# Kernel optimization log

Measured on AMD Instinct MI355X. Metric: run time of the kernel, lower is better.

The kernel has to match this reference:

```python
import jax, jax.numpy as jnp
import numpy as np

B, Q, C = 64, 512, 128   # batch, num_queries, num_activity_classes
P, G = 2048, 256         # num_persons, num_target_groups
COST_BCE = 1.0
COST_ACT = 1.0


def setup_inputs() -> dict:
    key = jax.random.key(0)
    k1, k2, k3, k4 = jax.random.split(key, 4)
    pred_activity_logits = jax.random.normal(k1, (B, Q, C), dtype=jnp.float32)
    attention_weights = jax.random.normal(k2, (B, P, Q), dtype=jnp.float32)
    # binary one-hot-style grouping targets (~each person in 1-of-G groups; sparse 0/1)
    tgt_one_hot = (jax.random.uniform(k3, (B, P, G)) < (1.0 / G) * 8).astype(jnp.float32)
    tgt_activity_ids = jax.random.randint(k4, (B, G), 0, C, dtype=jnp.int64)
    return {
        "pred_activity_logits": pred_activity_logits,
        "attention_weights": attention_weights,
        "tgt_one_hot": tgt_one_hot,
        "tgt_activity_ids": tgt_activity_ids,
    }


def reference(pred_activity_logits, attention_weights, tgt_one_hot, tgt_activity_ids):
    """Fused cost-matrix computation.

    BCEWithLogits(x, t) (mean reduction) = mean(softplus(x) - x * t).
    grouping_cost[b,i,j] = mean_p BCE(attw[b,p,i], onehot[b,p,j])
                         = mean_p softplus(attw[b,p,i]) - (1/P) sum_p attw[b,p,i]*onehot[b,p,j]
    activity_cost[b,i,j] = mean_c BCE(logits[b,i,c], onehot(ids[b,j])[c])
                         = mean_c softplus(logits[b,i,c]) - (1/C) * logits[b,i,ids[b,j]]
    Returns the [B, Q, G] cost tensor (scipy linear_sum_assignment, which consumes
    it on CPU, is outside the kernel scope).
    """
    attw = attention_weights            # [B, P, Q]
    logits = pred_activity_logits       # [B, Q, C]
    p = attw.shape[1]
    c = logits.shape[2]

    # grouping (BCE) cost
    sp_g = jnp.mean(jax.nn.softplus(attw), axis=1)               # [B, Q]
    xt = jnp.einsum('bpq,bpg->bqg', attw, tgt_one_hot) / p       # [B, Q, G]
    grouping_cost = sp_g[:, :, None] - xt                        # [B, Q, G]

    # activity (BCE vs one-hot class) cost
    sp_a = jnp.mean(jax.nn.softplus(logits), axis=2)             # [B, Q]
    idx = jnp.broadcast_to(tgt_activity_ids[:, None, :], (logits.shape[0], logits.shape[1], tgt_activity_ids.shape[1]))
    gathered = jnp.take_along_axis(logits, idx.astype(jnp.int32), axis=2)  # [B, Q, G]
    activity_cost = sp_a[:, :, None] - gathered / c              # [B, Q, G]

    cost = COST_BCE * grouping_cost + COST_ACT * activity_cost
    return cost
```

## Files before the change

### kernel.cpp

```cpp
#include <hip/hip_runtime.h>
#include <hip/hip_bf16.h>

#define B_  64
#define Q_  512
#define C_  128
#define P_  2048
#define G_  256
#define BM  128
#define BN  256
#define BK  64
#define NT  512

typedef __attribute__((ext_vector_type(8))) short short8;
typedef __attribute__((ext_vector_type(4))) float floatx4;

union FragU { uint4 u; short8 s; };

__device__ __forceinline__ float bf2f(unsigned short h) {
    union { unsigned int i; float f; } v; v.i = ((unsigned int)h) << 16; return v.f;
}
__device__ __forceinline__ unsigned int f2bf(float f) {
    union { float f; unsigned int u; } v; v.f = f;
    return (v.u + 0x7FFFu + ((v.u >> 16) & 1u)) >> 16;
}
__device__ __forceinline__ float splus(float x) {
    return fmaxf(x, 0.f) + __logf(1.f + __expf(-fabsf(x)));
}
__device__ __forceinline__ void unpack8(float4 a, float4 b, float* c) {
    c[0] = a.x; c[1] = a.y; c[2] = a.z; c[3] = a.w;
    c[4] = b.x; c[5] = b.y; c[6] = b.z; c[7] = b.w;
}

__global__ __launch_bounds__(NT, 2)
void fused_cost_kernel(const float* __restrict__ logits,
                       const float* __restrict__ attw,
                       const float* __restrict__ onehot,
                       const int* __restrict__ ids,
                       float* __restrict__ out)
{
    __shared__ unsigned short smem[(BM + BN) * BK];
    __shared__ float spq[BM];
    __shared__ int idt[BN];
    __shared__ int sflags;
    unsigned short* As = smem;
    unsigned short* Bs = smem + BM * BK;

    const int tid = threadIdx.x;
    const int l   = tid & 63;
    const int w   = tid >> 6;
    const int wm  = w & 1;
    const int wn  = w >> 1;
    const int lm  = l & 15;
    const int lk  = l >> 4;

    const int nb = blockIdx.x * BN;
    const int mb = blockIdx.y * BM;
    const int b  = blockIdx.z;

    if (tid < BM) spq[tid] = 0.f;
    if (tid == 0) sflags = 0;
    __syncthreads();
    if (tid < 128) { if (ids[2 * tid + 1] != 0) atomicOr(&sflags, 1); }
    __syncthreads();
    const bool ids32 = (sflags & 1) != 0;
    if (tid < BN) {
        const int gidx = b * G_ + nb + tid;
        idt[tid] = ids32 ? ids[gidx] : ids[2 * gidx];
    }

    const int mvA = tid & 15;
    const int kqA = tid >> 4;
    const int hbA = kqA >> 2;
    const int kdA = kqA & 3;
    const int mvB = tid & 31;
    const int kqB = tid >> 5;
    const int hbB = kqB >> 1;
    const int sdB = (kqB & 1) * 4;

    const float* aSrc = attw   + (size_t)b * P_ * Q_ + (size_t)(2 * kqA) * Q_ + (mb + 8 * mvA);
    const float* bSrc = onehot + (size_t)b * P_ * G_ + (size_t)(4 * kqB) * G_ + (nb + 8 * mvB);

    float spacc[8] = {0.f, 0.f, 0.f, 0.f, 0.f, 0.f, 0.f, 0.f};
    floatx4 acc[4][4];
    #pragma unroll
    for (int mi = 0; mi < 4; ++mi)
        #pragma unroll
        for (int ni = 0; ni < 4; ++ni)
            acc[mi][ni] = (floatx4){0.f, 0.f, 0.f, 0.f};

    float4 rA0 = *(const float4*)(aSrc);
    float4 rA1 = *(const float4*)(aSrc + 4);
    float4 rA2 = *(const float4*)(aSrc + Q_);
    float4 rA3 = *(const float4*)(aSrc + Q_ + 4);
    float4 rB0 = *(const float4*)(bSrc);
    float4 rB1 = *(const float4*)(bSrc + 4);
    float4 rB2 = *(const float4*)(bSrc + G_);
    float4 rB3 = *(const float4*)(bSrc + G_ + 4);
    float4 rB4 = *(const float4*)(bSrc + 2 * G_);
    float4 rB5 = *(const float4*)(bSrc + 2 * G_ + 4);
    float4 rB6 = *(const float4*)(bSrc + 3 * G_);
    float4 rB7 = *(const float4*)(bSrc + 3 * G_ + 4);

    for (int kb = 0; kb < P_; kb += BK) {
        __syncthreads();
        {
            float c0[8], c1[8];
            unpack8(rA0, rA1, c0);
            unpack8(rA2, rA3, c1);
            #pragma unroll
            for (int j = 0; j < 8; ++j) {
                spacc[j] += splus(c0[j]) + splus(c1[j]);
                const unsigned int d = f2bf(c0[j]) | (f2bf(c1[j]) << 16);
                const int m  = 8 * mvA + j;
                const int sw = (m + (m >> 3)) & 7;
                *(unsigned int*)(&As[m * BK + ((hbA ^ sw) << 3) + 2 * kdA]) = d;
            }
        }
        {
            float c0[8], c1[8], c2[8], c3[8];
            unpack8(rB0, rB1, c0);
            unpack8(rB2, rB3, c1);
            unpack8(rB4, rB5, c2);
            unpack8(rB6, rB7, c3);
            #pragma unroll
            for (int j = 0; j < 8; ++j) {
                uint2 dv;
                dv.x = f2bf(c0[j]) | (f2bf(c1[j]) << 16);
                dv.y = f2bf(c2[j]) | (f2bf(c3[j]) << 16);
                const int n  = 8 * mvB + j;
                const int sw = (n + (n >> 3)) & 7;
                *(uint2*)(&Bs[n * BK + ((hbB ^ sw) << 3) + sdB]) = dv;
            }
        }
        if (kb + BK < P_) {
            const float* an = aSrc + (size_t)(kb + BK) * Q_;
            const float* bn = bSrc + (size_t)(kb + BK) * G_;
            rA0 = *(const float4*)(an);
            rA1 = *(const float4*)(an + 4);
            rA2 = *(const float4*)(an + Q_);
            rA3 = *(const float4*)(an + Q_ + 4);
            rB0 = *(const float4*)(bn);
            rB1 = *(const float4*)(bn + 4);
            rB2 = *(const float4*)(bn + G_);
            rB3 = *(const float4*)(bn + G_ + 4);
            rB4 = *(const float4*)(bn + 2 * G_);
            rB5 = *(const float4*)(bn + 2 * G_ + 4);
            rB6 = *(const float4*)(bn + 3 * G_);
            rB7 = *(const float4*)(bn + 3 * G_ + 4);
        }
        __syncthreads();
        #pragma unroll
        for (int s = 0; s < 2; ++s) {
            FragU a4[4], b4[4];
            #pragma unroll
            for (int mi = 0; mi < 4; ++mi) {
                const int m  = 64 * wm + 16 * mi + lm;
                const int sw = (m + (m >> 3)) & 7;
                a4[mi].u = *(const uint4*)(&As[m * BK + (((4 * s + lk) ^ sw) << 3)]);
            }
            #pragma unroll
            for (int ni = 0; ni < 4; ++ni) {
                const int n  = 64 * wn + 16 * ni + lm;
                const int sw = (n + (n >> 3)) & 7;
                b4[ni].u = *(const uint4*)(&Bs[n * BK + (((4 * s + lk) ^ sw) << 3)]);
            }
            #pragma unroll
            for (int mi = 0; mi < 4; ++mi)
                #pragma unroll
                for (int ni = 0; ni < 4; ++ni)
                    acc[mi][ni] = __builtin_amdgcn_mfma_f32_16x16x32_bf16(
                        a4[mi].s, b4[ni].s, acc[mi][ni], 0, 0, 0);
        }
    }

    #pragma unroll
    for (int j = 0; j < 8; ++j)
        atomicAdd(&spq[8 * mvA + j], spacc[j] * (1.0f / P_));

    __syncthreads();

    {
        const int q  = tid >> 2;
        const int qt = tid & 3;
        const float4* src = (const float4*)(logits + ((size_t)b * Q_ + (mb + q)) * C_ + 32 * qt);
        uint2* dst = (uint2*)(&smem[q * C_ + 32 * qt]);
        float ssum = 0.f;
        #pragma unroll
        for (int i = 0; i < 8; ++i) {
            float4 t = src[i];
            ssum += splus(t.x) + splus(t.y) + splus(t.z) + splus(t.w);
            uint2 dv;
            dv.x = f2bf(t.x) | (f2bf(t.y) << 16);
            dv.y = f2bf(t.z) | (f2bf(t.w) << 16);
            dst[i] = dv;
        }
        atomicAdd(&spq[q], ssum * (1.0f / C_));
    }
    __syncthreads();

    float* outp = out + ((size_t)b * Q_ + mb) * G_ + nb;
    #pragma unroll
    for (int mi = 0; mi < 4; ++mi) {
        const int q0 = 64 * wm + 16 * mi + 4 * lk;
        #pragma unroll
        for (int ni = 0; ni < 4; ++ni) {
            const int g   = 64 * wn + 16 * ni + lm;
            const int cid = idt[g];
            #pragma unroll
            for (int r = 0; r < 4; ++r) {
                const int q = q0 + r;
                const float val = spq[q]
                                - acc[mi][ni][r] * (1.0f / P_)
                                - bf2f(smem[q * C_ + cid]) * (1.0f / C_);
                outp[(size_t)q * G_ + g] = val;
            }
        }
    }
}

extern "C" void kernel_launch(void* const* d_in, const int* in_sizes, int n_in,
                              void* d_out, int out_size, void* d_ws, size_t ws_size,
                              hipStream_t stream) {
    const float* logits = (const float*)d_in[0];
    const float* attw   = (const float*)d_in[1];
    const float* onehot = (const float*)d_in[2];
    const int*   ids    = (const int*)d_in[3];
    float*       out    = (float*)d_out;

    dim3 grid(G_ / BN, Q_ / BM, B_);
    hipLaunchKernelGGL(fused_cost_kernel, grid, dim3(NT), 0, stream,
                       logits, attw, onehot, ids, out);
}
```

Baseline: 477.8 us.

## Double-buffer LDS tiles to drop one barrier per K-step, truncate onehot bf16

```diff
diff --git a/kernel.cpp b/kernel.cpp
--- a/kernel.cpp
+++ b/kernel.cpp
@@ -10,6 +10,8 @@
 #define BN  256
 #define BK  64
 #define NT  512
+#define NTILES (P_ / BK)
+#define HALF ((BM + BN) * BK)
 
 typedef __attribute__((ext_vector_type(8))) short short8;
 typedef __attribute__((ext_vector_type(4))) float floatx4;
@@ -19,9 +21,12 @@
 __device__ __forceinline__ float bf2f(unsigned short h) {
     union { unsigned int i; float f; } v; v.i = ((unsigned int)h) << 16; return v.f;
 }
+__device__ __forceinline__ unsigned int fbits(float f) {
+    union { float f; unsigned int u; } v; v.f = f; return v.u;
+}
 __device__ __forceinline__ unsigned int f2bf(float f) {
-    union { float f; unsigned int u; } v; v.f = f;
-    return (v.u + 0x7FFFu + ((v.u >> 16) & 1u)) >> 16;
+    unsigned int u = fbits(f);
+    return (u + 0x7FFFu + ((u >> 16) & 1u)) >> 16;
 }
 __device__ __forceinline__ float splus(float x) {
     return fmaxf(x, 0.f) + __logf(1.f + __expf(-fabsf(x)));
@@ -38,12 +43,10 @@
                        const int* __restrict__ ids,
                        float* __restrict__ out)
 {
-    __shared__ unsigned short smem[(BM + BN) * BK];
+    __shared__ unsigned short smem[2 * HALF];
     __shared__ float spq[BM];
     __shared__ int idt[BN];
     __shared__ int sflags;
-    unsigned short* As = smem;
-    unsigned short* Bs = smem + BM * BK;
 
     const int tid = threadIdx.x;
     const int l   = tid & 63;
@@ -77,8 +80,8 @@
     const int hbB = kqB >> 1;
     const int sdB = (kqB & 1) * 4;
 
-    const float* aSrc = attw   + (size_t)b * P_ * Q_ + (size_t)(2 * kqA) * Q_ + (mb + 8 * mvA);
-    const float* bSrc = onehot + (size_t)b * P_ * G_ + (size_t)(4 * kqB) * G_ + (nb + 8 * mvB);
+    const float* aBase = attw   + (size_t)b * P_ * Q_ + (size_t)(2 * kqA) * Q_ + (mb + 8 * mvA);
+    const float* bBase = onehot + (size_t)b * P_ * G_ + (size_t)(4 * kqB) * G_ + (nb + 8 * mvB);
 
     float spacc[8] = {0.f, 0.f, 0.f, 0.f, 0.f, 0.f, 0.f, 0.f};
     floatx4 acc[4][4];
@@ -88,21 +91,24 @@
         for (int ni = 0; ni < 4; ++ni)
             acc[mi][ni] = (floatx4){0.f, 0.f, 0.f, 0.f};
 
-    float4 rA0 = *(const float4*)(aSrc);
-    float4 rA1 = *(const float4*)(aSrc + 4);
-    float4 rA2 = *(const float4*)(aSrc + Q_);
-    float4 rA3 = *(const float4*)(aSrc + Q_ + 4);
-    float4 rB0 = *(const float4*)(bSrc);
-    float4 rB1 = *(const float4*)(bSrc + 4);
-    float4 rB2 = *(const float4*)(bSrc + G_);
-    float4 rB3 = *(const float4*)(bSrc + G_ + 4);
-    float4 rB4 = *(const float4*)(bSrc + 2 * G_);
-    float4 rB5 = *(const float4*)(bSrc + 2 * G_ + 4);
-    float4 rB6 = *(const float4*)(bSrc + 3 * G_);
-    float4 rB7 = *(const float4*)(bSrc + 3 * G_ + 4);
-
-    for (int kb = 0; kb < P_; kb += BK) {
-        __syncthreads();
+    float4 rA0 = *(const float4*)(aBase);
+    float4 rA1 = *(const float4*)(aBase + 4);
+    float4 rA2 = *(const float4*)(aBase + Q_);
+    float4 rA3 = *(const float4*)(aBase + Q_ + 4);
+    float4 rB0 = *(const float4*)(bBase);
+    float4 rB1 = *(const float4*)(bBase + 4);
+    float4 rB2 = *(const float4*)(bBase + G_);
+    float4 rB3 = *(const float4*)(bBase + G_ + 4);
+    float4 rB4 = *(const float4*)(bBase + 2 * G_);
+    float4 rB5 = *(const float4*)(bBase + 2 * G_ + 4);
+    float4 rB6 = *(const float4*)(bBase + 3 * G_);
+    float4 rB7 = *(const float4*)(bBase + 3 * G_ + 4);
+
+    #pragma unroll 2
+    for (int t = 0; t < NTILES; ++t) {
+        unsigned short* As = smem + (t & 1) * HALF;
+        unsigned short* Bs = As + BM * BK;
+
         {
             float c0[8], c1[8];
             unpack8(rA0, rA1, c0);
@@ -125,16 +131,16 @@
             #pragma unroll
             for (int j = 0; j < 8; ++j) {
                 uint2 dv;
-                dv.x = f2bf(c0[j]) | (f2bf(c1[j]) << 16);
-                dv.y = f2bf(c2[j]) | (f2bf(c3[j]) << 16);
+                dv.x = (fbits(c0[j]) >> 16) | (fbits(c1[j]) & 0xFFFF0000u);
+                dv.y = (fbits(c2[j]) >> 16) | (fbits(c3[j]) & 0xFFFF0000u);
                 const int n  = 8 * mvB + j;
                 const int sw = (n + (n >> 3)) & 7;
                 *(uint2*)(&Bs[n * BK + ((hbB ^ sw) << 3) + sdB]) = dv;
             }
         }
-        if (kb + BK < P_) {
-            const float* an = aSrc + (size_t)(kb + BK) * Q_;
-            const float* bn = bSrc + (size_t)(kb + BK) * G_;
+        if (t + 1 < NTILES) {
+            const float* an = aBase + (size_t)(t + 1) * BK * Q_;
+            const float* bn = bBase + (size_t)(t + 1) * BK * G_;
             rA0 = *(const float4*)(an);
             rA1 = *(const float4*)(an + 4);
             rA2 = *(const float4*)(an + Q_);
@@ -148,7 +154,9 @@
             rB6 = *(const float4*)(bn + 3 * G_);
             rB7 = *(const float4*)(bn + 3 * G_ + 4);
         }
+        __builtin_amdgcn_sched_barrier(0);
         __syncthreads();
+
         #pragma unroll
         for (int s = 0; s < 2; ++s) {
             FragU a4[4], b4[4];
```

Result: slower. 502.6 us (+5.2%).
